# Performance work log

Measured on AMD Instinct MI355X. Metric: run time of the kernel, lower is better.

Reference implementation:

```python
import jax, jax.numpy as jnp
from jax import lax
import numpy as np

B = 2048; IMG = 28; K = 3; CIN = 1; HC = 32; LC = 16; WID = 64; HID = 64
LIS = IMG - 3 * (K - 1)           # 22: latent image size
FLAT = LIS * LIS * HC             # 15488
BLK = WID * LC                    # 1024: hypernet block size
T1 = 10.0; T0 = 0.0; NSTEP = 20   # fixed-step RK4 replaces adaptive dopri5
VAR = 0.1                         # p_z0 diagonal covariance


def _conv(x, w, b):  # w: [Cout,Cin,k,k], VALID conv, stride 1
    y = lax.conv_general_dilated(x, w, (1, 1), 'VALID',
                                 dimension_numbers=('NCHW', 'OIHW', 'NCHW'))
    return y + b[None, :, None, None]


def _convT(x, w, b):  # w: [Cin,Cout,k,k] (pytorch ConvTranspose2d layout)
    wf = jnp.flip(w, (2, 3)).transpose(1, 0, 2, 3)  # -> OIHW, spatially flipped
    y = lax.conv_general_dilated(x, wf, (1, 1), [(K - 1, K - 1), (K - 1, K - 1)],
                                 dimension_numbers=('NCHW', 'OIHW', 'NCHW'))
    return y + b[None, :, None, None]


def _forward(x, c0w, c0b, c1w, c1b, c2w, c2b, elw, elb, dlw, dlb,
             t0w, t0b, t1w, t1b, t2w, t2b, h1w, h1b, h2w, h2b, h3w, h3b):
    # ---- encoder (dropout in eval = identity) ----
    h = jnp.tanh(_conv(x, c0w, c0b))
    h = jnp.tanh(_conv(h, c1w, c1b))
    h = jnp.tanh(_conv(h, c2w, c2b))
    z1 = h.reshape(h.shape[0], -1) @ elw + elb          # [B, LC]
    # ---- decoder ----
    d = jnp.tanh(z1 @ dlw + dlb)                         # [B, FLAT]
    d = d.reshape(-1, HC, LIS, LIS)
    d = jnp.tanh(_convT(d, t0w, t0b))
    d = jnp.tanh(_convT(d, t1w, t1b))
    recon = _convT(d, t2w, t2b)                          # [B, CIN, 28, 28]

    # ---- CNF vector field with analytic trace ----
    def hyper(t):
        p = jnp.tanh(jnp.reshape(jnp.asarray(t, jnp.float32), (1, 1)) @ h1w + h1b)
        p = jnp.tanh(p @ h2w + h2b)
        p = (p @ h3w + h3b).reshape(-1)
        W = p[:BLK].reshape(WID, LC)
        U = p[BLK:2 * BLK].reshape(WID, LC) * jax.nn.sigmoid(p[2 * BLK:3 * BLK].reshape(WID, LC))
        Bb = p[3 * BLK:]                                 # [WID]
        return W, Bb, U

    def f(t, z):
        W, Bb, U = hyper(t)
        hh = jnp.tanh(jnp.einsum('bd,wd->wb', z, W) + Bb[:, None])   # [WID, B]
        dz = jnp.einsum('wb,wd->bd', hh, U) / WID                     # [B, LC]
        s = jnp.sum(W * U, axis=1)                                    # [WID]: sum_i W_w[i]U_w[i]
        tr = jnp.mean((1.0 - hh * hh) * s[:, None], axis=0)           # [B] analytic trace
        return dz, -tr[:, None]

    dt = (T0 - T1) / NSTEP

    def step(state, i):
        z, lp = state
        t = T1 + i * dt
        k1z, k1l = f(t, z)
        k2z, k2l = f(t + 0.5 * dt, z + 0.5 * dt * k1z)
        k3z, k3l = f(t + 0.5 * dt, z + 0.5 * dt * k2z)
        k4z, k4l = f(t + dt, z + dt * k3z)
        z = z + dt / 6.0 * (k1z + 2 * k2z + 2 * k3z + k4z)
        lp = lp + dt / 6.0 * (k1l + 2 * k2l + 2 * k3l + k4l)
        return (z, lp), None

    lp1 = jnp.zeros((z1.shape[0], 1), z1.dtype)
    (z0, lp0), _ = lax.scan(step, (z1, lp1), jnp.arange(NSTEP, dtype=jnp.float32))

    # MultivariateNormal(0, 0.1*I) log_prob
    logp = -0.5 * (LC * jnp.log(2 * jnp.pi) + LC * jnp.log(VAR) + jnp.sum(z0 * z0, -1) / VAR)
    x_probs = jnp.mean(logp - lp0[:, 0])
    return recon, x_probs


def setup_inputs() -> dict:
    key = jax.random.key(0)
    ks = jax.random.split(key, 16)
    n = jax.random.normal
    s = jnp.float32(0.05)
    z = jnp.zeros
    OUT3 = 3 * BLK + WID
    return {
        'x': n(ks[0], (B, CIN, IMG, IMG), jnp.float32),
        'c0w': n(ks[1], (HC, CIN, K, K)) * s, 'c0b': z((HC,)),
        'c1w': n(ks[2], (HC, HC, K, K)) * s, 'c1b': z((HC,)),
        'c2w': n(ks[3], (HC, HC, K, K)) * s, 'c2b': z((HC,)),
        'elw': n(ks[4], (FLAT, LC)) * s, 'elb': z((LC,)),
        'dlw': n(ks[5], (LC, FLAT)) * s, 'dlb': z((FLAT,)),
        't0w': n(ks[6], (HC, HC, K, K)) * s, 't0b': z((HC,)),
        't1w': n(ks[7], (HC, HC, K, K)) * s, 't1b': z((HC,)),
        't2w': n(ks[8], (HC, CIN, K, K)) * s, 't2b': z((CIN,)),
        'h1w': n(ks[9], (1, HID)) * s, 'h1b': z((HID,)),
        'h2w': n(ks[10], (HID, HID)) * s, 'h2b': z((HID,)),
        'h3w': n(ks[11], (HID, OUT3)) * s, 'h3b': z((OUT3,)),
    }


def reference(x, c0w, c0b, c1w, c1b, c2w, c2b, elw, elb, dlw, dlb,
              t0w, t0b, t1w, t1b, t2w, t2b, h1w, h1b, h2w, h2b, h3w, h3b):
    return _forward(x, c0w, c0b, c1w, c1b, c2w, c2b, elw, elb, dlw, dlb,
                    t0w, t0b, t1w, t1b, t2w, t2b, h1w, h1b, h2w, h2b, h3w, h3b)
```

## Files before the change

### kernel.cpp

```cpp
#include <hip/hip_runtime.h>
#include <math.h>

#define Bsz 2048

using bf16x8 = __attribute__((ext_vector_type(8))) short;
using f32x4  = __attribute__((ext_vector_type(4))) float;

__device__ __forceinline__ float fast_tanh(float x){
    float e = __expf(2.0f * x);
    return 1.0f - 2.0f / (e + 1.0f);
}
__device__ __forceinline__ float fast_sigmoid(float x){
    return 1.0f / (1.0f + __expf(-x));
}
__device__ __forceinline__ unsigned short f2b(float f){
    union { float f; unsigned u; } v; v.f = f;
    unsigned r = v.u + 0x7FFFu + ((v.u >> 16) & 1u);
    return (unsigned short)(r >> 16);
}
__device__ __forceinline__ float b2f(unsigned short s){
    union { unsigned u; float f; } v; v.u = ((unsigned)s) << 16;
    return v.f;
}

__device__ __forceinline__ float stage_t(int sidx){
    int i  = sidx >> 2, st = sidx & 3;
    float t = 10.0f - 0.5f * (float)i;
    if (st == 1 || st == 2) t -= 0.25f;
    else if (st == 3)       t -= 0.5f;
    return t;
}

__global__ void k_prep(const float* __restrict__ c1w, const float* __restrict__ c2w,
                       const float* __restrict__ t0w, const float* __restrict__ t1w,
                       const float* __restrict__ elw, const float* __restrict__ dlw,
                       const float* __restrict__ elb,
                       unsigned short* __restrict__ wc1, unsigned short* __restrict__ wc2,
                       unsigned short* __restrict__ wt0, unsigned short* __restrict__ wt1,
                       unsigned short* __restrict__ elwT, unsigned short* __restrict__ dlwT,
                       float* __restrict__ z1, int full){
    int gsz = gridDim.x * 256;
    for (int i = blockIdx.x*256 + threadIdx.x; i < 9216; i += gsz){
        int ci = i & 31, co = (i >> 5) & 31, s = i >> 10;
        wc1[i] = f2b(c1w[(co*32 + ci)*9 + s]);
        wc2[i] = f2b(c2w[(co*32 + ci)*9 + s]);
        wt0[i] = f2b(t0w[(ci*32 + co)*9 + (8 - s)]);
        wt1[i] = f2b(t1w[(ci*32 + co)*9 + (8 - s)]);
    }
    if (!full) return;
    for (int i = blockIdx.x*256 + threadIdx.x; i < 32768; i += gsz)
        z1[i] = elb[i & 15];
    for (int i = blockIdx.x*256 + threadIdx.x; i < 247808; i += gsz){
        int l = i / 15488, f2 = i - l*15488;
        int pos = f2 >> 5, ci = f2 & 31;
        elwT[i] = f2b(elw[(ci*484 + pos)*16 + l]);
    }
    for (int i = blockIdx.x*256 + threadIdx.x; i < 247808; i += gsz){
        int f2 = i >> 4, l = i & 15;
        int pos = f2 >> 5, ci = f2 & 31;
        dlwT[i] = f2b(dlw[l*15488 + ci*484 + pos]);
    }
}

__global__ void __launch_bounds__(256)
k_conv0(const float* __restrict__ x, const float* __restrict__ c0w,
        const float* __restrict__ c0b, unsigned short* __restrict__ A0,
        int cb, int CH){
    int gid = blockIdx.x*256 + threadIdx.x;
    if (gid >= CH*676) return;
    int b = gid / 676, pos = gid - b*676;
    int y = pos / 26, xx = pos - y*26;
    const float* xin = x + (size_t)(cb + b)*784;
    float v[9];
#pragma unroll
    for (int r = 0; r < 3; r++)
#pragma unroll
        for (int s = 0; s < 3; s++)
            v[r*3+s] = xin[(y+r)*28 + xx + s];
    unsigned short* ob = A0 + (size_t)b*21632 + pos*32;
#pragma unroll
    for (int g = 0; g < 8; g++){
        float a0 = c0b[g*4+0], a1 = c0b[g*4+1], a2 = c0b[g*4+2], a3 = c0b[g*4+3];
#pragma unroll
        for (int k = 0; k < 9; k++){
            a0 += v[k] * c0w[(g*4+0)*9 + k];
            a1 += v[k] * c0w[(g*4+1)*9 + k];
            a2 += v[k] * c0w[(g*4+2)*9 + k];
            a3 += v[k] * c0w[(g*4+3)*9 + k];
        }
        ushort4 o;
        o.x = f2b(fast_tanh(a0)); o.y = f2b(fast_tanh(a1));
        o.z = f2b(fast_tanh(a2)); o.w = f2b(fast_tanh(a3));
        *(ushort4*)(ob + g*4) = o;
    }
}

template<int IL, int OL, int OW, int OOFF, int INS, int OUTS>
__global__ void __launch_bounds__(256)
k_convM(const unsigned short* __restrict__ in, const unsigned short* __restrict__ wg,
        const float* __restrict__ bias, unsigned short* __restrict__ out, int CH){
    constexpr int N  = OL * OL;
    constexpr int NT = (N + 15) / 16;
    const int tid = threadIdx.x;
    const int wave = tid >> 6, lane = tid & 63;
    const int q = lane >> 4, nn = lane & 15;
    const int nw = gridDim.x * 4;

    bf16x8 af[2][9];
#pragma unroll
    for (int mt = 0; mt < 2; mt++)
#pragma unroll
        for (int s = 0; s < 9; s++)
            af[mt][s] = *(const bf16x8*)(wg + s*1024 + (mt*16 + nn)*32 + q*8);
    float4 bc0 = *(const float4*)(bias + q*4);
    float4 bc1 = *(const float4*)(bias + 16 + q*4);

    for (int t = blockIdx.x*4 + wave; t < CH*NT; t += nw){
        int img = t / NT, tt = t - img*NT;
        const unsigned short* inb = in + (size_t)img * INS;
        unsigned short* outb = out + (size_t)img * OUTS;
        int pos = tt*16 + nn;
        int pc  = pos < N ? pos : N - 1;
        int oy = pc / OL, ox = pc - oy*OL;
        const unsigned short* ib = inb + (oy*IL + ox)*32 + q*8;
        f32x4 acc0 = {0.f,0.f,0.f,0.f}, acc1 = {0.f,0.f,0.f,0.f};
#pragma unroll
        for (int r = 0; r < 3; r++){
            bf16x8 b0 = *(const bf16x8*)(ib + (r*IL + 0)*32);
            bf16x8 b1 = *(const bf16x8*)(ib + (r*IL + 1)*32);
            bf16x8 b2 = *(const bf16x8*)(ib + (r*IL + 2)*32);
            acc0 = __builtin_amdgcn_mfma_f32_16x16x32_bf16(af[0][r*3+0], b0, acc0, 0,0,0);
            acc1 = __builtin_amdgcn_mfma_f32_16x16x32_bf16(af[1][r*3+0], b0, acc1, 0,0,0);
            acc0 = __builtin_amdgcn_mfma_f32_16x16x32_bf16(af[0][r*3+1], b1, acc0, 0,0,0);
            acc1 = __builtin_amdgcn_mfma_f32_16x16x32_bf16(af[1][r*3+1], b1, acc1, 0,0,0);
            acc0 = __builtin_amdgcn_mfma_f32_16x16x32_bf16(af[0][r*3+2], b2, acc0, 0,0,0);
            acc1 = __builtin_amdgcn_mfma_f32_16x16x32_bf16(af[1][r*3+2], b2, acc1, 0,0,0);
        }
        if (pos < N){
            int opix = oy*OW + ox + OOFF;
            ushort4 o0, o1;
            o0.x = f2b(fast_tanh(acc0[0] + bc0.x)); o0.y = f2b(fast_tanh(acc0[1] + bc0.y));
            o0.z = f2b(fast_tanh(acc0[2] + bc0.z)); o0.w = f2b(fast_tanh(acc0[3] + bc0.w));
            o1.x = f2b(fast_tanh(acc1[0] + bc1.x)); o1.y = f2b(fast_tanh(acc1[1] + bc1.y));
            o1.z = f2b(fast_tanh(acc1[2] + bc1.z)); o1.w = f2b(fast_tanh(acc1[3] + bc1.w));
            *(ushort4*)(outb + opix*32 + q*4)      = o0;
            *(ushort4*)(outb + opix*32 + 16 + q*4) = o1;
        }
    }
}

__global__ void __launch_bounds__(256)
k_encg(const unsigned short* __restrict__ A2, const unsigned short* __restrict__ elwT,
       float* __restrict__ z1, int cb, int CH){
    int wave = threadIdx.x >> 6, lane = threadIdx.x & 63;
    int q = lane >> 4, nn = lane & 15;
    int imgb = blockIdx.x*16;
    const unsigned short* ap = A2 + (size_t)(imgb + nn)*15488 + q*8;
    const unsigned short* bp = elwT + (size_t)nn*15488 + q*8;
    f32x4 acc = {0.f,0.f,0.f,0.f};
    int s0 = blockIdx.y*121;
#pragma unroll 2
    for (int s = s0 + wave; s < s0 + 121; s += 4){
        bf16x8 a = *(const bf16x8*)(ap + s*32);
        bf16x8 b = *(const bf16x8*)(bp + s*32);
        acc = __builtin_amdgcn_mfma_f32_16x16x32_bf16(a, b, acc, 0,0,0);
    }
    float* zp = z1 + (size_t)(cb + imgb)*16;
#pragma unroll
    for (int i = 0; i < 4; i++)
        atomicAdd(zp + (q*4 + i)*16 + nn, acc[i]);
}

__global__ void __launch_bounds__(256)
k_halo(unsigned short* __restrict__ D0, unsigned short* __restrict__ D1, int CH){
    int gid = blockIdx.x*256 + threadIdx.x;
    uint4 zq = {0,0,0,0};
    if (gid < CH*676){
        int img = gid / 676, px = gid - img*676;
        int y = px / 26, x = px - y*26;
        if (y < 2 || y >= 24 || x < 2 || x >= 24){
            uint4* p = (uint4*)(D0 + (size_t)img*21632 + px*32);
            p[0] = zq; p[1] = zq; p[2] = zq; p[3] = zq;
        }
    } else {
        int g2 = gid - CH*676;
        if (g2 >= CH*784) return;
        int img = g2 / 784, px = g2 - img*784;
        int y = px / 28, x = px - y*28;
        if (y < 2 || y >= 26 || x < 2 || x >= 26){
            uint4* p = (uint4*)(D1 + (size_t)img*25088 + px*32);
            p[0] = zq; p[1] = zq; p[2] = zq; p[3] = zq;
        }
    }
}

__global__ void __launch_bounds__(256)
k_decg(const float* __restrict__ z1, const unsigned short* __restrict__ dlwT,
       const float* __restrict__ dlb, unsigned short* __restrict__ D0,
       int cb, int CH){
    __shared__ float zl[256];
    int tid = threadIdx.x, ib = blockIdx.y;
    zl[tid] = z1[(size_t)(cb + ib*16 + (tid >> 4))*16 + (tid & 15)];
    __syncthreads();
    int ci = tid & 31, po = tid >> 5;
    int pos = blockIdx.x*8 + po;
    if (pos >= 484) return;
    int y = pos / 22, xx = pos - y*22;
    float bias = dlb[ci*484 + pos];
    const unsigned short* w = dlwT + (size_t)(pos*32 + ci)*16;
    bf16x8 w0 = *(const bf16x8*)(w);
    bf16x8 w1 = *(const bf16x8*)(w + 8);
    float wf[16];
#pragma unroll
    for (int j = 0; j < 8; j++){
        wf[j]   = b2f((unsigned short)w0[j]);
        wf[8+j] = b2f((unsigned short)w1[j]);
    }
    int opix = ((y+2)*26 + xx + 2)*32 + ci;
#pragma unroll 1
    for (int i = 0; i < 16; i++){
        float a = bias;
#pragma unroll
        for (int l = 0; l < 16; l++) a += zl[i*16 + l] * wf[l];
        D0[(size_t)(ib*16 + i)*21632 + opix] = f2b(fast_tanh(a));
    }
}

__global__ void __launch_bounds__(256)
k_convT2(const unsigned short* __restrict__ D2, const float* __restrict__ t2w,
         const float* __restrict__ t2b, float* __restrict__ out, int cb, int CH){
    int gid = blockIdx.x*256 + threadIdx.x;
    if (gid >= CH*784) return;
    int b = gid / 784, o = gid - b*784;
    int y = o / 28, xx = o - y*28;
    const unsigned short* db = D2 + (size_t)b*21632;
    float a = t2b[0];
#pragma unroll
    for (int r = 0; r < 3; r++){
        int iy = y + r - 2;
        if ((unsigned)iy >= 26u) continue;
#pragma unroll
        for (int s = 0; s < 3; s++){
            int ix = xx + s - 2;
            if ((unsigned)ix >= 26u) continue;
            const unsigned short* pp = db + (iy*26 + ix)*32;
            int wi = (2-r)*3 + (2-s);
#pragma unroll
            for (int g = 0; g < 4; g++){
                bf16x8 h = *(const bf16x8*)(pp + g*8);
#pragma unroll
                for (int j = 0; j < 8; j++)
                    a += b2f((unsigned short)h[j]) * t2w[(g*8+j)*9 + wi];
            }
        }
    }
    out[(size_t)(cb + b)*784 + o] = a;
}

template<int LOUT, int INW, int OUTW, int OUTOFF>
__device__ __forceinline__ void conv_gemm(const unsigned short* __restrict__ Wg,
                                          const float* __restrict__ bias,
                                          const unsigned short* inL,
                                          unsigned short* outL, int tid){
    constexpr int N  = LOUT * LOUT;
    constexpr int NT = (N + 15) / 16;
    const int lane  = tid & 63;
    const int wave  = tid >> 6;
    const int mtile = wave & 1;
    const int quad  = lane >> 4;
    const int nn    = lane & 15;
    bf16x8 afr[9];
    const unsigned short* wp = Wg + (mtile*16 + nn)*32 + quad*8;
#pragma unroll
    for (int s = 0; s < 9; s++)
        afr[s] = *(const bf16x8*)(wp + s*1024);
    float4 bco = *(const float4*)(bias + mtile*16 + quad*4);
    for (int t = (wave >> 1); t < NT; t += 2){
        int pos = t*16 + nn;
        int pc  = pos < N ? pos : N - 1;
        int y = pc / LOUT, x = pc - y*LOUT;
        const unsigned short* ib = inL + (y*INW + x)*32 + quad*8;
        f32x4 acc = {0.f, 0.f, 0.f, 0.f};
#pragma unroll
        for (int r = 0; r < 3; r++)
#pragma unroll
            for (int s = 0; s < 3; s++)
                acc = __builtin_amdgcn_mfma_f32_16x16x32_bf16(
                        afr[r*3+s], *(const bf16x8*)(ib + (r*INW + s)*32), acc, 0, 0, 0);
        if (pos < N){
            ushort4 o;
            o.x = f2b(fast_tanh(acc[0] + bco.x));
            o.y = f2b(fast_tanh(acc[1] + bco.y));
            o.z = f2b(fast_tanh(acc[2] + bco.z));
            o.w = f2b(fast_tanh(acc[3] + bco.w));
            int opix = y*OUTW + x + OUTOFF;
            *(ushort4*)(outL + opix*32 + mtile*16 + quad*4) = o;
        }
    }
}

__global__ void __launch_bounds__(256)
k_enc_f(const float* __restrict__ x,
        const float* __restrict__ c0w, const float* __restrict__ c0b,
        const unsigned short* __restrict__ wc1, const float* __restrict__ c1b,
        const unsigned short* __restrict__ wc2, const float* __restrict__ c2b,
        const float* __restrict__ elw, const float* __restrict__ elb,
        float* __restrict__ z1){
    __shared__ float X[784];
    __shared__ __align__(16) unsigned short H0[21632];
    __shared__ __align__(16) unsigned short H1[18432];
    __shared__ __align__(16) unsigned short H2[15488];
    __shared__ float red[16*17];
    const int tid = threadIdx.x, b = blockIdx.x;
    for (int i = tid; i < 784; i += 256) X[i] = x[b*784 + i];
    __syncthreads();
    for (int pos = tid; pos < 676; pos += 256){
        int y = pos / 26, xx = pos - y*26;
        float v[9];
#pragma unroll
        for (int r = 0; r < 3; r++)
#pragma unroll
            for (int s = 0; s < 3; s++)
                v[r*3+s] = X[(y+r)*28 + xx + s];
#pragma unroll
        for (int g = 0; g < 8; g++){
            float a0 = c0b[g*4+0], a1 = c0b[g*4+1], a2 = c0b[g*4+2], a3 = c0b[g*4+3];
#pragma unroll
            for (int k = 0; k < 9; k++){
                a0 += v[k] * c0w[(g*4+0)*9 + k];
                a1 += v[k] * c0w[(g*4+1)*9 + k];
                a2 += v[k] * c0w[(g*4+2)*9 + k];
                a3 += v[k] * c0w[(g*4+3)*9 + k];
            }
            ushort4 o;
            o.x = f2b(fast_tanh(a0)); o.y = f2b(fast_tanh(a1));
            o.z = f2b(fast_tanh(a2)); o.w = f2b(fast_tanh(a3));
            *(ushort4*)(H0 + pos*32 + g*4) = o;
        }
    }
    __syncthreads();
    conv_gemm<24, 26, 24, 0>(wc1, c1b, H0, H1, tid);
    __syncthreads();
    conv_gemm<22, 24, 22, 0>(wc2, c2b, H1, H2, tid);
    __syncthreads();
    {
        int fg = tid >> 4, l = tid & 15;
        float a = 0.f;
        for (int ci = 0; ci < 32; ci++)
            for (int pos = fg; pos < 484; pos += 16)
                a += b2f(H2[pos*32 + ci]) * elw[(ci*484 + pos)*16 + l];
        red[fg*17 + l] = a;
        __syncthreads();
        if (tid < 16){
            float s = elb[tid];
#pragma unroll
            for (int g = 0; g < 16; g++) s += red[g*17 + tid];
            z1[b*16 + tid] = s;
        }
    }
}

__global__ void __launch_bounds__(256)
k_dec_f(const float* __restrict__ z1,
        const float* __restrict__ dlw, const float* __restrict__ dlb,
        const unsigned short* __restrict__ wt0, const float* __restrict__ t0b,
        const unsigned short* __restrict__ wt1, const float* __restrict__ t1b,
        const float* __restrict__ t2w, const float* __restrict__ t2b,
        float* __restrict__ out){
    __shared__ __align__(16) unsigned short D0[21632];
    __shared__ __align__(16) unsigned short D1[25088];
    __shared__ __align__(16) unsigned short D2[28800];
    const int tid = threadIdx.x, b = blockIdx.x;
    {
        uint4 zq = {0,0,0,0};
        for (int i = tid; i < 2704; i += 256) ((uint4*)D0)[i] = zq;
        for (int i = tid; i < 3136; i += 256) ((uint4*)D1)[i] = zq;
        for (int i = tid; i < 3600; i += 256) ((uint4*)D2)[i] = zq;
    }
    float zz[16];
#pragma unroll
    for (int l = 0; l < 16; l++) zz[l] = z1[b*16 + l];
    __syncthreads();
    for (int f = tid; f < 15488; f += 256){
        float a = dlb[f];
#pragma unroll
        for (int l = 0; l < 16; l++) a += zz[l] * dlw[l*15488 + f];
        int ci = f / 484, pos = f - ci*484;
        int y = pos / 22, xx = pos - y*22;
        D0[((y+2)*26 + xx + 2)*32 + ci] = f2b(fast_tanh(a));
    }
    __syncthreads();
    conv_gemm<24, 26, 28, 58>(wt0, t0b, D0, D1, tid);
    __syncthreads();
    conv_gemm<26, 28, 30, 62>(wt1, t1b, D1, D2, tid);
    __syncthreads();
    for (int o = tid; o < 784; o += 256){
        int y = o / 28, xx = o - y*28;
        float a = t2b[0];
#pragma unroll
        for (int r = 0; r < 3; r++)
#pragma unroll
            for (int s = 0; s < 3; s++){
                const unsigned short* pp = D2 + ((y+r)*30 + xx + s)*32;
                int wi = (2-r)*3 + (2-s);
#pragma unroll
                for (int g = 0; g < 4; g++){
                    bf16x8 h = *(const bf16x8*)(pp + g*8);
#pragma unroll
                    for (int j = 0; j < 8; j++)
                        a += b2f((unsigned short)h[j]) * t2w[(g*8+j)*9 + wi];
                }
            }
        out[(size_t)b*784 + o] = a;
    }
}

__global__ void __launch_bounds__(64)
k_hyp1(const float* __restrict__ h1w, const float* __restrict__ h1b,
       const float* __restrict__ h2w, const float* __restrict__ h2b,
       float* __restrict__ p2ws){
    __shared__ float p1l[64];
    int sidx = blockIdx.x, tid = threadIdx.x;
    float t = stage_t(sidx);
    p1l[tid] = fast_tanh(t * h1w[tid] + h1b[tid]);
    __syncthreads();
    float a0 = h2b[tid], a1 = 0.f, a2 = 0.f, a3 = 0.f;
#pragma unroll
    for (int k = 0; k < 64; k += 4){
        a0 += p1l[k]   * h2w[(k)*64   + tid];
        a1 += p1l[k+1] * h2w[(k+1)*64 + tid];
        a2 += p1l[k+2] * h2w[(k+2)*64 + tid];
        a3 += p1l[k+3] * h2w[(k+3)*64 + tid];
    }
    p2ws[sidx*64 + tid] = fast_tanh((a0 + a1) + (a2 + a3));
}

__global__ void __launch_bounds__(256)
k_hyp2(const float* __restrict__ p2ws, const float* __restrict__ h3w,
       const float* __restrict__ h3b, float* __restrict__ p3ws){
    __shared__ float p2l[64];
    int sidx = blockIdx.y, tid = threadIdx.x;
    if (tid < 64) p2l[tid] = p2ws[sidx*64 + tid];
    __syncthreads();
    int m = blockIdx.x*256 + tid;
    if (m >= 3136) return;
    const float* hp = h3w + m;
    float a0 = h3b[m], a1 = 0.f, a2 = 0.f, a3 = 0.f;
#pragma unroll
    for (int k = 0; k < 64; k += 4){
        a0 += p2l[k]   * hp[(size_t)(k)*3136];
        a1 += p2l[k+1] * hp[(size_t)(k+1)*3136];
        a2 += p2l[k+2] * hp[(size_t)(k+2)*3136];
        a3 += p2l[k+3] * hp[(size_t)(k+3)*3136];
    }
    p3ws[(size_t)sidx*3200 + m] = (a0 + a1) + (a2 + a3);
}

__global__ void __launch_bounds__(256)
k_hyp3(const float* __restrict__ p3ws, float* __restrict__ hyp){
    __shared__ float sred[64];
    int sidx = blockIdx.x, tid = threadIdx.x;
    const float* p3 = p3ws + (size_t)sidx*3200;
    float* g = hyp + (size_t)sidx*2048;
    unsigned short* gW = (unsigned short*)g;
    unsigned short* gU = (unsigned short*)(g + 1024);

    {
        int lane = tid & 63, c = tid >> 6;
        int q = lane >> 4, m = lane & 15;
        ushort4 o0 = {0,0,0,0}, o1 = {0,0,0,0};
        if (q < 2){
            const float* wp = p3 + (c*16 + m)*16 + q*8;
            o0.x = f2b(wp[0]); o0.y = f2b(wp[1]); o0.z = f2b(wp[2]); o0.w = f2b(wp[3]);
            o1.x = f2b(wp[4]); o1.y = f2b(wp[5]); o1.z = f2b(wp[6]); o1.w = f2b(wp[7]);
        }
        *(ushort4*)(gW + tid*8)     = o0;
        *(ushort4*)(gW + tid*8 + 4) = o1;
    }
    if (tid < 128){
        int lane = tid & 63, kb = tid >> 6;
        int q = lane >> 4, d = lane & 15;
        unsigned short uo[8];
#pragma unroll
        for (int j = 0; j < 8; j++){
            int w = kb*32 + q*8 + j;
            float u = p3[1024 + w*16 + d] * fast_sigmoid(p3[2048 + w*16 + d]);
            uo[j] = f2b(u);
        }
        *(ushort4*)(gU + tid*8)     = *(ushort4*)&uo[0];
        *(ushort4*)(gU + tid*8 + 4) = *(ushort4*)&uo[4];
    } else if (tid < 192){
        int w = tid - 128;
        g[1536 + w] = p3[3072 + w];
    } else {
        int w = tid - 192;
        float s = 0.f;
#pragma unroll
        for (int d = 0; d < 16; d++){
            float u = p3[1024 + w*16 + d] * fast_sigmoid(p3[2048 + w*16 + d]);
            s += p3[w*16 + d] * u;
        }
        g[1600 + w] = s;
        sred[w] = s;
    }
    __syncthreads();
    if (tid == 0){
        float st = 0.f;
#pragma unroll
        for (int w = 0; w < 64; w++) st += sred[w];
        g[1664] = st;
    }
}

__global__ void k_hyper(const float* __restrict__ h1w, const float* __restrict__ h1b,
                        const float* __restrict__ h2w, const float* __restrict__ h2b,
                        const float* __restrict__ h3w, const float* __restrict__ h3b,
                        float* __restrict__ hyp){
    int sidx = blockIdx.x;
    float t = stage_t(sidx);
    __shared__ float p1[64], p2[64];
    __shared__ float p3[3136];
    int tid = threadIdx.x;
    if (tid < 64) p1[tid] = fast_tanh(t * h1w[tid] + h1b[tid]);
    __syncthreads();
    if (tid < 64){
        float a = h2b[tid];
#pragma unroll
        for (int k = 0; k < 64; k++) a += p1[k] * h2w[k*64 + tid];
        p2[tid] = fast_tanh(a);
    }
    __syncthreads();
    for (int m = tid; m < 3136; m += 256){
        float a = h3b[m];
#pragma unroll
        for (int k = 0; k < 64; k++) a += p2[k] * h3w[k*3136 + m];
        p3[m] = a;
    }
    __syncthreads();
    float* g = hyp + (size_t)sidx * 2304;
    for (int m = tid; m < 1024; m += 256){
        g[m] = p3[m];
        float u = p3[1024 + m] * fast_sigmoid(p3[2048 + m]);
        g[1024 + (m & 15)*64 + (m >> 4)] = u;
        p3[1024 + m] = u;
    }
    if (tid < 64) g[2048 + tid] = p3[3072 + tid];
    __syncthreads();
    if (tid < 64){
        float s = 0.f;
#pragma unroll
        for (int d = 0; d < 16; d++) s += p3[tid*16 + d] * p3[1024 + tid*16 + d];
        g[2112 + tid] = s;
    }
}

struct PM {
    bf16x8 Wf[4];
    bf16x8 Uf[2];
    float4 Bbf[4];
    float4 sf[4];
    float stot;
};
__device__ __forceinline__ void loadPM(const float* __restrict__ g, int lane, int q, PM& p){
    const unsigned short* gW = (const unsigned short*)g;
    const unsigned short* gU = (const unsigned short*)(g + 1024);
#pragma unroll
    for (int c = 0; c < 4; c++)
        p.Wf[c] = *(const bf16x8*)(gW + (c*64 + lane)*8);
#pragma unroll
    for (int kb = 0; kb < 2; kb++)
        p.Uf[kb] = *(const bf16x8*)(gU + (kb*64 + lane)*8);
#pragma unroll
    for (int c = 0; c < 4; c++){
        p.Bbf[c] = *(const float4*)(g + 1536 + c*16 + q*4);
        p.sf[c]  = *(const float4*)(g + 1600 + c*16 + q*4);
    }
    p.stot = g[1664];
}

__global__ void __launch_bounds__(64)
k_cnfM(const float* __restrict__ z1, const float* __restrict__ hyp,
       float* __restrict__ part){
    __shared__ __align__(16) float zsf[384];
    __shared__ __align__(16) unsigned short hhT[16*72];
    __shared__ float trl[16];
    const int lane = threadIdx.x;
    const int q = lane >> 4, d = lane & 15;
    const float dt = -0.5f;

    float z[4], zacc[4], lacc[4], lp[4];
#pragma unroll
    for (int i = 0; i < 4; i++){
        z[i] = z1[(size_t)(blockIdx.x*16 + q*4 + i)*16 + d];
        zacc[i] = 0.f; lacc[i] = 0.f; lp[i] = 0.f;
        zsf[(q*4 + i)*20 + d] = z[i];
    }
    PM cur, nxt;
    loadPM(hyp, lane, q, cur);

    for (int sidx = 0; sidx < 80; sidx++){
        bf16x8 zb;
        if (q < 2){
            float4 za = *(const float4*)(zsf + d*20 + q*8);
            float4 zc = *(const float4*)(zsf + d*20 + q*8 + 4);
            zb[0]=(short)f2b(za.x); zb[1]=(short)f2b(za.y);
            zb[2]=(short)f2b(za.z); zb[3]=(short)f2b(za.w);
            zb[4]=(short)f2b(zc.x); zb[5]=(short)f2b(zc.y);
            zb[6]=(short)f2b(zc.z); zb[7]=(short)f2b(zc.w);
        } else {
            bf16x8 zz2 = {0,0,0,0,0,0,0,0}; zb = zz2;
        }
        f32x4 h0 = {0,0,0,0}, h1 = {0,0,0,0}, h2 = {0,0,0,0}, h3 = {0,0,0,0};
        h0 = __builtin_amdgcn_mfma_f32_16x16x32_bf16(cur.Wf[0], zb, h0, 0,0,0);
        h1 = __builtin_amdgcn_mfma_f32_16x16x32_bf16(cur.Wf[1], zb, h1, 0,0,0);
        h2 = __builtin_amdgcn_mfma_f32_16x16x32_bf16(cur.Wf[2], zb, h2, 0,0,0);
        h3 = __builtin_amdgcn_mfma_f32_16x16x32_bf16(cur.Wf[3], zb, h3, 0,0,0);
        if (sidx < 79) loadPM(hyp + (size_t)(sidx + 1)*2048, lane, q, nxt);

        float partial = 0.f;
        f32x4 hc[4] = {h0, h1, h2, h3};
#pragma unroll
        for (int c = 0; c < 4; c++){
            ushort4 o;
            float t0 = fast_tanh(hc[c][0] + cur.Bbf[c].x);
            float t1 = fast_tanh(hc[c][1] + cur.Bbf[c].y);
            float t2 = fast_tanh(hc[c][2] + cur.Bbf[c].z);
            float t3 = fast_tanh(hc[c][3] + cur.Bbf[c].w);
            partial += t0*t0*cur.sf[c].x + t1*t1*cur.sf[c].y
                     + t2*t2*cur.sf[c].z + t3*t3*cur.sf[c].w;
            o.x = f2b(t0); o.y = f2b(t1); o.z = f2b(t2); o.w = f2b(t3);
            *(ushort4*)(hhT + d*72 + c*16 + q*4) = o;
        }
        partial += __shfl_xor(partial, 16);
        partial += __shfl_xor(partial, 32);
        if (lane < 16) trl[lane] = (cur.stot - partial) * (1.f/64.f);

        bf16x8 a20 = *(const bf16x8*)(hhT + d*72 + q*8);
        bf16x8 a21 = *(const bf16x8*)(hhT + d*72 + 32 + q*8);
        f32x4 dzac = {0,0,0,0};
        dzac = __builtin_amdgcn_mfma_f32_16x16x32_bf16(a20, cur.Uf[0], dzac, 0,0,0);
        dzac = __builtin_amdgcn_mfma_f32_16x16x32_bf16(a21, cur.Uf[1], dzac, 0,0,0);

        int st = sidx & 3;
        float wgt = (st == 0 || st == 3) ? 1.f : 2.f;
#pragma unroll
        for (int i = 0; i < 4; i++){
            float dz = dzac[i] * (1.f/64.f);
            float dl = -trl[q*4 + i];
            zacc[i] += wgt * dz;
            lacc[i] += wgt * dl;
            float zsv;
            if (st < 3){
                float aa = (st == 2) ? 1.0f : 0.5f;
                zsv = z[i] + aa * dt * dz;
            } else {
                z[i]  += (dt/6.f) * zacc[i];
                lp[i] += (dt/6.f) * lacc[i];
                zsv = z[i];
                zacc[i] = 0.f; lacc[i] = 0.f;
            }
            zsf[(q*4 + i)*20 + d] = zsv;
        }
        cur = nxt;
    }
    float sq[4];
#pragma unroll
    for (int i = 0; i < 4; i++) sq[i] = z[i]*z[i];
#pragma unroll
    for (int off = 1; off < 16; off <<= 1){
#pragma unroll
        for (int i = 0; i < 4; i++) sq[i] += __shfl_xor(sq[i], off, 16);
    }
    if (d == 0){
#pragma unroll
        for (int i = 0; i < 4; i++){
            float logp = -0.5f * (16.f*1.8378770664093453f
                                 + 16.f*(-2.302585092994046f) + sq[i]*10.f);
            part[blockIdx.x*16 + q*4 + i] = logp - lp[i];
        }
    }
}

struct PF { float4 Wr[4]; float4 Ur[4]; float Bb, sw; };
__device__ __forceinline__ void load_pf(const float* __restrict__ g,
                                        int lane, int q, int d, PF& p){
    const float4* w4 = (const float4*)(g + lane*16);
    p.Wr[0] = w4[0]; p.Wr[1] = w4[1]; p.Wr[2] = w4[2]; p.Wr[3] = w4[3];
    const float4* u4 = (const float4*)(g + 1024 + d*64 + q*16);
    p.Ur[0] = u4[0]; p.Ur[1] = u4[1]; p.Ur[2] = u4[2]; p.Ur[3] = u4[3];
    p.Bb = g[2048 + lane];
    p.sw = g[2112 + lane];
}
__global__ void __launch_bounds__(64)
k_cnf_f(const float* __restrict__ z1, const float* __restrict__ hyp,
        float* __restrict__ part){
    __shared__ __align__(16) float zsl[16];
    __shared__ __align__(16) float hhl[64];
    const int lane = threadIdx.x;
    const int q = lane >> 4, d = lane & 15;
    const float dt = -0.5f;
    float z  = z1[(size_t)blockIdx.x*16 + d];
    float zs = z;
    float lp = 0.f, zacc = 0.f, lacc = 0.f;
    if (lane < 16) zsl[lane] = zs;
    PF cur, nxt;
    load_pf(hyp, lane, q, d, cur);
    for (int sidx = 0; sidx < 80; sidx++){
        __syncthreads();
        if (sidx < 79) load_pf(hyp + (size_t)(sidx + 1)*2304, lane, q, d, nxt);
        const float4* zp = (const float4*)zsl;
        float4 z0 = zp[0], z1v = zp[1], z2 = zp[2], z3 = zp[3];
        float a = cur.Bb;
        a += z0.x*cur.Wr[0].x + z0.y*cur.Wr[0].y + z0.z*cur.Wr[0].z + z0.w*cur.Wr[0].w;
        a += z1v.x*cur.Wr[1].x + z1v.y*cur.Wr[1].y + z1v.z*cur.Wr[1].z + z1v.w*cur.Wr[1].w;
        a += z2.x*cur.Wr[2].x + z2.y*cur.Wr[2].y + z2.z*cur.Wr[2].z + z2.w*cur.Wr[2].w;
        a += z3.x*cur.Wr[3].x + z3.y*cur.Wr[3].y + z3.z*cur.Wr[3].z + z3.w*cur.Wr[3].w;
        float hh = fast_tanh(a);
        float e = (1.f - hh*hh) * cur.sw;
#pragma unroll
        for (int off = 1; off < 64; off <<= 1)
            e += __shfl_xor(e, off);
        hhl[lane] = hh;
        __syncthreads();
        const float4* hp = (const float4*)(hhl + q*16);
        float4 h0 = hp[0], h1 = hp[1], h2 = hp[2], h3 = hp[3];
        float dzp = 0.f;
        dzp += h0.x*cur.Ur[0].x + h0.y*cur.Ur[0].y + h0.z*cur.Ur[0].z + h0.w*cur.Ur[0].w;
        dzp += h1.x*cur.Ur[1].x + h1.y*cur.Ur[1].y + h1.z*cur.Ur[1].z + h1.w*cur.Ur[1].w;
        dzp += h2.x*cur.Ur[2].x + h2.y*cur.Ur[2].y + h2.z*cur.Ur[2].z + h2.w*cur.Ur[2].w;
        dzp += h3.x*cur.Ur[3].x + h3.y*cur.Ur[3].y + h3.z*cur.Ur[3].z + h3.w*cur.Ur[3].w;
        dzp += __shfl_xor(dzp, 16);
        dzp += __shfl_xor(dzp, 32);
        float dz = dzp * (1.f/64.f);
        float dl = -e  * (1.f/64.f);
        int st = sidx & 3;
        float wgt = (st == 0 || st == 3) ? 1.f : 2.f;
        zacc += wgt * dz;
        lacc += wgt * dl;
        if (st < 3){
            float aa = (st == 2) ? 1.0f : 0.5f;
            zs = z + aa * dt * dz;
        } else {
            z  += (dt/6.f) * zacc;
            lp += (dt/6.f) * lacc;
            zs = z;
            zacc = 0.f; lacc = 0.f;
        }
        if (lane < 16) zsl[lane] = zs;
        cur = nxt;
    }
    float sq = z * z;
#pragma unroll
    for (int off = 1; off < 16; off <<= 1) sq += __shfl_xor(sq, off, 16);
    float logp = -0.5f * (16.f*1.8378770664093453f + 16.f*(-2.302585092994046f) + sq*10.f);
    if (lane == 0) part[blockIdx.x] = logp - lp;
}

__global__ void k_final(const float* __restrict__ part, float* __restrict__ out){
    __shared__ float red[256];
    int tid = threadIdx.x;
    float s = 0.f;
#pragma unroll
    for (int k = 0; k < 8; k++) s += part[tid + k*256];
    red[tid] = s;
    __syncthreads();
    for (int st = 128; st > 0; st >>= 1){
        if (tid < st) red[tid] += red[tid + st];
        __syncthreads();
    }
    if (tid == 0) out[1605632] = red[0] * (1.f/2048.f);
}

extern "C" void kernel_launch(void* const* d_in, const int* in_sizes, int n_in,
                              void* d_out, int out_size, void* d_ws, size_t ws_size,
                              hipStream_t stream){
    const float* x   = (const float*)d_in[0];
    const float* c0w = (const float*)d_in[1];
    const float* c0b = (const float*)d_in[2];
    const float* c1w = (const float*)d_in[3];
    const float* c1b = (const float*)d_in[4];
    const float* c2w = (const float*)d_in[5];
    const float* c2b = (const float*)d_in[6];
    const float* elw = (const float*)d_in[7];
    const float* elb = (const float*)d_in[8];
    const float* dlw = (const float*)d_in[9];
    const float* dlb = (const float*)d_in[10];
    const float* t0w = (const float*)d_in[11];
    const float* t0b = (const float*)d_in[12];
    const float* t1w = (const float*)d_in[13];
    const float* t1b = (const float*)d_in[14];
    const float* t2w = (const float*)d_in[15];
    const float* t2b = (const float*)d_in[16];
    const float* h1w = (const float*)d_in[17];
    const float* h1b = (const float*)d_in[18];
    const float* h2w = (const float*)d_in[19];
    const float* h2b = (const float*)d_in[20];
    const float* h3w = (const float*)d_in[21];
    const float* h3b = (const float*)d_in[22];

    float* ws   = (float*)d_ws;
    float* z1   = ws;
    float* hyp  = z1 + 32768;
    float* part = hyp + 184320;
    float* p2ws = part + 2048;
    float* p3ws = p2ws + 5120;
    unsigned short* wc1  = (unsigned short*)(p3ws + 256000);
    unsigned short* wc2  = wc1 + 9216;
    unsigned short* wt0  = wc2 + 9216;
    unsigned short* wt1  = wt0 + 9216;
    unsigned short* elwT = wt1 + 9216;
    unsigned short* dlwT = elwT + 247808;
    unsigned short* act  = dlwT + 247808;
    float* rec  = (float*)d_out;

    const size_t MISC = 2985984;
    int CH = 0;
    const int cands[6] = {2048, 1024, 512, 256, 128, 64};
    for (int c = 0; c < 6; c++){
        size_t need = MISC + (size_t)cands[c] * 111104;
        if (need <= ws_size){ CH = cands[c]; break; }
    }

    if (CH == 0){
        k_hyper<<<80, 256, 0, stream>>>(h1w, h1b, h2w, h2b, h3w, h3b, hyp);
        k_prep <<<64,   256, 0, stream>>>(c1w, c2w, t0w, t1w, elw, dlw, elb,
                                          wc1, wc2, wt0, wt1, wt1, wt1, z1, 0);
        k_enc_f<<<2048, 256, 0, stream>>>(x, c0w, c0b, wc1, c1b, wc2, c2b, elw, elb, z1);
        k_cnf_f<<<2048,  64, 0, stream>>>(z1, hyp, part);
        k_dec_f<<<2048, 256, 0, stream>>>(z1, dlw, dlb, wt0, t0b, wt1, t1b, t2w, t2b, rec);
        k_final<<<1,    256, 0, stream>>>(part, rec);
        return;
    }

    k_hyp1<<<80,           64, 0, stream>>>(h1w, h1b, h2w, h2b, p2ws);
    k_hyp2<<<dim3(13,80), 256, 0, stream>>>(p2ws, h3w, h3b, p3ws);
    k_hyp3<<<80,          256, 0, stream>>>(p3ws, hyp);

    k_prep<<<64, 256, 0, stream>>>(c1w, c2w, t0w, t1w, elw, dlw, elb,
                                   wc1, wc2, wt0, wt1, elwT, dlwT, z1, 1);

    unsigned short* R0 = act;
    unsigned short* R1 = R0 + (size_t)CH*21632;
    unsigned short* R2 = R1 + (size_t)CH*18432;
    unsigned short* D1 = R1;

    for (int cb = 0; cb < Bsz; cb += CH){
        k_conv0<<<(CH*676 + 255)/256, 256, 0, stream>>>(x, c0w, c0b, R0, cb, CH);
        k_convM<26,24,24, 0, 21632, 18432><<<(CH*36 + 15)/16, 256, 0, stream>>>(R0, wc1, c1b, R1, CH);
        k_convM<24,22,22, 0, 18432, 15488><<<(CH*31 + 15)/16, 256, 0, stream>>>(R1, wc2, c2b, R2, CH);
        k_encg<<<dim3(CH/16, 4), 256, 0, stream>>>(R2, elwT, z1, cb, CH);
        k_halo<<<(CH*1460 + 255)/256, 256, 0, stream>>>(R0, D1, CH);
        k_decg<<<dim3(61, CH/16), 256, 0, stream>>>(z1, dlwT, dlb, R0, cb, CH);
        k_convM<26,24,28,58, 21632, 25088><<<(CH*36 + 15)/16, 256, 0, stream>>>(R0, wt0, t0b, D1, CH);
        k_convM<28,26,26, 0, 25088, 21632><<<(CH*43 + 15)/16, 256, 0, stream>>>(D1, wt1, t1b, R0, CH);
        k_convT2<<<(CH*784 + 255)/256, 256, 0, stream>>>(R0, t2w, t2b, rec, cb, CH);
    }
    k_cnfM <<<128,  64, 0, stream>>>(z1, hyp, part);
    k_final<<<1,   256, 0, stream>>>(part, rec);
}
```

Before: 652.2 us.

## Fold halo zeroing into decoder GEMM, ping-pong activations, bf16 z staging in CNF

Removes the separate halo-zeroing kernel and runs that work in five extra blocks of the decoder linear kernel. Activation buffers are cut to two ping-pong regions, which lowers the per-chunk workspace need and may allow a larger chunk size. In the CNF kernel, z is stored in LDS as bf16 so the per-step conversion is gone, the trace value is passed by shuffle instead of through LDS, and the hypernet parameters are double-buffered by reference instead of copied each step. It also issues the next-step parameter load earlier.

```diff
diff --git a/kernel.cpp b/kernel.cpp
--- a/kernel.cpp
+++ b/kernel.cpp
@@ -155,7 +155,7 @@
     int wave = threadIdx.x >> 6, lane = threadIdx.x & 63;
     int q = lane >> 4, nn = lane & 15;
     int imgb = blockIdx.x*16;
-    const unsigned short* ap = A2 + (size_t)(imgb + nn)*15488 + q*8;
+    const unsigned short* ap = A2 + (size_t)(imgb + nn)*21632 + q*8;
     const unsigned short* bp = elwT + (size_t)nn*15488 + q*8;
     f32x4 acc = {0.f,0.f,0.f,0.f};
     int s0 = blockIdx.y*121;
@@ -172,36 +172,34 @@
 }
 
 __global__ void __launch_bounds__(256)
-k_halo(unsigned short* __restrict__ D0, unsigned short* __restrict__ D1, int CH){
-    int gid = blockIdx.x*256 + threadIdx.x;
-    uint4 zq = {0,0,0,0};
-    if (gid < CH*676){
-        int img = gid / 676, px = gid - img*676;
-        int y = px / 26, x = px - y*26;
-        if (y < 2 || y >= 24 || x < 2 || x >= 24){
-            uint4* p = (uint4*)(D0 + (size_t)img*21632 + px*32);
-            p[0] = zq; p[1] = zq; p[2] = zq; p[3] = zq;
-        }
-    } else {
-        int g2 = gid - CH*676;
-        if (g2 >= CH*784) return;
-        int img = g2 / 784, px = g2 - img*784;
-        int y = px / 28, x = px - y*28;
-        if (y < 2 || y >= 26 || x < 2 || x >= 26){
-            uint4* p = (uint4*)(D1 + (size_t)img*25088 + px*32);
-            p[0] = zq; p[1] = zq; p[2] = zq; p[3] = zq;
-        }
-    }
-}
-
-__global__ void __launch_bounds__(256)
 k_decg(const float* __restrict__ z1, const unsigned short* __restrict__ dlwT,
        const float* __restrict__ dlb, unsigned short* __restrict__ D0,
-       int cb, int CH){
+       unsigned short* __restrict__ D1, int cb, int CH){
     __shared__ float zl[256];
     int tid = threadIdx.x, ib = blockIdx.y;
     zl[tid] = z1[(size_t)(cb + ib*16 + (tid >> 4))*16 + (tid & 15)];
     __syncthreads();
+    if (blockIdx.x >= 61){
+        int hid = (blockIdx.x - 61)*256 + tid;
+        uint4 zq = {0,0,0,0};
+        for (int p = hid; p < 16*676; p += 1280){
+            int im = p / 676, px = p - im*676;
+            int y = px / 26, x = px - y*26;
+            if (y < 2 || y >= 24 || x < 2 || x >= 24){
+                uint4* pt = (uint4*)(D0 + (size_t)(ib*16 + im)*21632 + px*32);
+                pt[0] = zq; pt[1] = zq; pt[2] = zq; pt[3] = zq;
+            }
+        }
+        for (int p = hid; p < 16*784; p += 1280){
+            int im = p / 784, px = p - im*784;
+            int y = px / 28, x = px - y*28;
+            if (y < 2 || y >= 26 || x < 2 || x >= 26){
+                uint4* pt = (uint4*)(D1 + (size_t)(ib*16 + im)*25088 + px*32);
+                pt[0] = zq; pt[1] = zq; pt[2] = zq; pt[3] = zq;
+            }
+        }
+        return;
+    }
     int ci = tid & 31, po = tid >> 5;
     int pos = blockIdx.x*8 + po;
     if (pos >= 484) return;
@@ -581,9 +579,8 @@
 __global__ void __launch_bounds__(64)
 k_cnfM(const float* __restrict__ z1, const float* __restrict__ hyp,
        float* __restrict__ part){
-    __shared__ __align__(16) float zsf[384];
+    __shared__ __align__(16) unsigned short zsb[16*24];
     __shared__ __align__(16) unsigned short hhT[16*72];
-    __shared__ float trl[16];
     const int lane = threadIdx.x;
     const int q = lane >> 4, d = lane & 15;
     const float dt = -0.5f;
@@ -593,29 +590,26 @@
     for (int i = 0; i < 4; i++){
         z[i] = z1[(size_t)(blockIdx.x*16 + q*4 + i)*16 + d];
         zacc[i] = 0.f; lacc[i] = 0.f; lp[i] = 0.f;
-        zsf[(q*4 + i)*20 + d] = z[i];
-    }
-    PM cur, nxt;
-    loadPM(hyp, lane, q, cur);
-
+        zsb[(q*4 + i)*24 + d] = f2b(z[i]);
+    }
+    PM pm0, pm1;
+    loadPM(hyp, lane, q, pm0);
+
+#pragma unroll 2
     for (int sidx = 0; sidx < 80; sidx++){
+        PM& cur = (sidx & 1) ? pm1 : pm0;
+        PM& nxt = (sidx & 1) ? pm0 : pm1;
+        if (sidx < 79) loadPM(hyp + (size_t)(sidx + 1)*2048, lane, q, nxt);
+
         bf16x8 zb;
-        if (q < 2){
-            float4 za = *(const float4*)(zsf + d*20 + q*8);
-            float4 zc = *(const float4*)(zsf + d*20 + q*8 + 4);
-            zb[0]=(short)f2b(za.x); zb[1]=(short)f2b(za.y);
-            zb[2]=(short)f2b(za.z); zb[3]=(short)f2b(za.w);
-            zb[4]=(short)f2b(zc.x); zb[5]=(short)f2b(zc.y);
-            zb[6]=(short)f2b(zc.z); zb[7]=(short)f2b(zc.w);
-        } else {
-            bf16x8 zz2 = {0,0,0,0,0,0,0,0}; zb = zz2;
-        }
+        if (q < 2) zb = *(const bf16x8*)(zsb + d*24 + q*8);
+        else { bf16x8 zz2 = {0,0,0,0,0,0,0,0}; zb = zz2; }
+
         f32x4 h0 = {0,0,0,0}, h1 = {0,0,0,0}, h2 = {0,0,0,0}, h3 = {0,0,0,0};
         h0 = __builtin_amdgcn_mfma_f32_16x16x32_bf16(cur.Wf[0], zb, h0, 0,0,0);
         h1 = __builtin_amdgcn_mfma_f32_16x16x32_bf16(cur.Wf[1], zb, h1, 0,0,0);
         h2 = __builtin_amdgcn_mfma_f32_16x16x32_bf16(cur.Wf[2], zb, h2, 0,0,0);
         h3 = __builtin_amdgcn_mfma_f32_16x16x32_bf16(cur.Wf[3], zb, h3, 0,0,0);
-        if (sidx < 79) loadPM(hyp + (size_t)(sidx + 1)*2048, lane, q, nxt);
 
         float partial = 0.f;
         f32x4 hc[4] = {h0, h1, h2, h3};
@@ -633,7 +627,7 @@
         }
         partial += __shfl_xor(partial, 16);
         partial += __shfl_xor(partial, 32);
-        if (lane < 16) trl[lane] = (cur.stot - partial) * (1.f/64.f);
+        float trFull = (cur.stot - partial) * (1.f/64.f);
 
         bf16x8 a20 = *(const bf16x8*)(hhT + d*72 + q*8);
         bf16x8 a21 = *(const bf16x8*)(hhT + d*72 + 32 + q*8);
@@ -646,7 +640,7 @@
 #pragma unroll
         for (int i = 0; i < 4; i++){
             float dz = dzac[i] * (1.f/64.f);
-            float dl = -trl[q*4 + i];
+            float dl = -__shfl(trFull, q*4 + i);
             zacc[i] += wgt * dz;
             lacc[i] += wgt * dl;
             float zsv;
@@ -659,9 +653,8 @@
                 zsv = z[i];
                 zacc[i] = 0.f; lacc[i] = 0.f;
             }
-            zsf[(q*4 + i)*20 + d] = zsv;
-        }
-        cur = nxt;
+            zsb[(q*4 + i)*24 + d] = f2b(zsv);
+        }
     }
     float sq[4];
 #pragma unroll
@@ -817,7 +810,7 @@
     int CH = 0;
     const int cands[6] = {2048, 1024, 512, 256, 128, 64};
     for (int c = 0; c < 6; c++){
-        size_t need = MISC + (size_t)cands[c] * 111104;
+        size_t need = MISC + (size_t)cands[c] * 93440;
         if (need <= ws_size){ CH = cands[c]; break; }
     }
 
@@ -839,21 +832,18 @@
     k_prep<<<64, 256, 0, stream>>>(c1w, c2w, t0w, t1w, elw, dlw, elb,
                                    wc1, wc2, wt0, wt1, elwT, dlwT, z1, 1);
 
-    unsigned short* R0 = act;
-    unsigned short* R1 = R0 + (size_t)CH*21632;
-    unsigned short* R2 = R1 + (size_t)CH*18432;
-    unsigned short* D1 = R1;
+    unsigned short* Y = act;
+    unsigned short* X = Y + (size_t)CH*21632;
 
     for (int cb = 0; cb < Bsz; cb += CH){
-        k_conv0<<<(CH*676 + 255)/256, 256, 0, stream>>>(x, c0w, c0b, R0, cb, CH);
-        k_convM<26,24,24, 0, 21632, 18432><<<(CH*36 + 15)/16, 256, 0, stream>>>(R0, wc1, c1b, R1, CH);
-        k_convM<24,22,22, 0, 18432, 15488><<<(CH*31 + 15)/16, 256, 0, stream>>>(R1, wc2, c2b, R2, CH);
-        k_encg<<<dim3(CH/16, 4), 256, 0, stream>>>(R2, elwT, z1, cb, CH);
-        k_halo<<<(CH*1460 + 255)/256, 256, 0, stream>>>(R0, D1, CH);
-        k_decg<<<dim3(61, CH/16), 256, 0, stream>>>(z1, dlwT, dlb, R0, cb, CH);
-        k_convM<26,24,28,58, 21632, 25088><<<(CH*36 + 15)/16, 256, 0, stream>>>(R0, wt0, t0b, D1, CH);
-        k_convM<28,26,26, 0, 25088, 21632><<<(CH*43 + 15)/16, 256, 0, stream>>>(D1, wt1, t1b, R0, CH);
-        k_convT2<<<(CH*784 + 255)/256, 256, 0, stream>>>(R0, t2w, t2b, rec, cb, CH);
+        k_conv0<<<(CH*676 + 255)/256, 256, 0, stream>>>(x, c0w, c0b, Y, cb, CH);
+        k_convM<26,24,24, 0, 21632, 25088><<<(CH*36 + 15)/16, 256, 0, stream>>>(Y, wc1, c1b, X, CH);
+        k_convM<24,22,22, 0, 25088, 21632><<<(CH*31 + 15)/16, 256, 0, stream>>>(X, wc2, c2b, Y, CH);
+        k_encg<<<dim3(CH/16, 4), 256, 0, stream>>>(Y, elwT, z1, cb, CH);
+        k_decg<<<dim3(66, CH/16), 256, 0, stream>>>(z1, dlwT, dlb, Y, X, cb, CH);
+        k_convM<26,24,28,58, 21632, 25088><<<(CH*36 + 15)/16, 256, 0, stream>>>(Y, wt0, t0b, X, CH);
+        k_convM<28,26,26, 0, 25088, 21632><<<(CH*43 + 15)/16, 256, 0, stream>>>(X, wt1, t1b, Y, CH);
+        k_convT2<<<(CH*784 + 255)/256, 256, 0, stream>>>(Y, t2w, t2b, rec, cb, CH);
     }
     k_cnfM <<<128,  64, 0, stream>>>(z1, hyp, part);
     k_final<<<1,   256, 0, stream>>>(part, rec);
```

Result: faster. 636.5 us (-2.4%).
